# Performance work log

Measured on AMD Instinct MI355X. Metric: run time of the kernel, lower is better.

The kernel has to match this reference:

```python
import jax, jax.numpy as jnp
import numpy as np

B, S, D, A, C, TT, T, NS = 64, 512, 1024, 128, 64, 32, 40, 64
NEG = -1e9


def setup_inputs() -> dict:
    key = jax.random.key(0)
    ks = jax.random.split(key, 24)
    n = lambda k, sh, s: jax.random.normal(k, sh, dtype=jnp.float32) * s
    inp = {
        "encoded_src": n(ks[0], (B, S, D), 1.0),
        "encoded_col": n(ks[1], (B, C, D), 1.0),
        "encoded_tab": n(ks[2], (B, TT, D), 1.0),
        "h0": n(ks[3], (B, D), 1.0),
        "c0": n(ks[4], (B, D), 1.0),
        "action_emb": n(ks[5], (A, D), 0.1),
        "symbol_emb": n(ks[6], (NS, D), 0.1),
        "W_tgt": n(ks[7], (D, D), 0.02), "b_tgt": jnp.zeros((D,), jnp.float32),
        "W_act": n(ks[8], (D, D), 0.02), "b_act": jnp.zeros((D,), jnp.float32),
        "W_col": n(ks[9], (D, D), 0.02), "b_col": jnp.zeros((D,), jnp.float32),
        "W_tab": n(ks[10], (D, D), 0.02), "b_tab": jnp.zeros((D,), jnp.float32),
        "W_out": n(ks[11], (D, D), 0.02), "b_out": jnp.zeros((D,), jnp.float32),
        "W_ih": n(ks[12], (3 * D, 4 * D), 0.02), "b_ih": jnp.zeros((4 * D,), jnp.float32),
        "W_hh": n(ks[13], (D, 4 * D), 0.02), "b_hh": jnp.zeros((4 * D,), jnp.float32),
        "src_mask": jnp.zeros((B, S), jnp.int32),
        "col_mask": jnp.zeros((B, C), jnp.int32),
        "tab_mask": jnp.zeros((B, TT), jnp.int32),
        "action_mask": jnp.zeros((B, A), jnp.int32),
        "cur_node_ids": jax.random.randint(ks[14], (T, B), 0, NS, dtype=jnp.int32),
        "kind": jax.random.randint(ks[15], (T, B), 0, 3, dtype=jnp.int32),
        "gold_idx": jax.random.randint(ks[16], (T, B), 0, TT, dtype=jnp.int32),
    }
    return inp


def reference(encoded_src, encoded_col, encoded_tab, h0, c0, action_emb, symbol_emb,
              W_tgt, b_tgt, W_act, b_act, W_col, b_col, W_tab, b_tab, W_out, b_out,
              W_ih, b_ih, W_hh, b_hh,
              src_mask, col_mask, tab_mask, action_mask, cur_node_ids, kind, gold_idx):
    dt = encoded_src.dtype
    nT, nB = cur_node_ids.shape
    nA = action_emb.shape[0]
    nC = encoded_col.shape[1]
    nTT = encoded_tab.shape[1]
    dim = encoded_src.shape[-1]

    # mask==1 means masked-out (matches torch code: allowed positions set to 0)
    src_bias = jnp.where(src_mask == 1, NEG, 0.0).astype(dt)
    act_bias = jnp.where(action_mask == 1, NEG, 0.0).astype(dt)
    col_bias = jnp.where(col_mask == 1, NEG, 0.0).astype(dt)
    tab_bias = jnp.where(tab_mask == 1, NEG, 0.0).astype(dt)

    # previous-action embedding per step: gather from action table / encoded cols / encoded tabs
    bidx = jnp.arange(nB)
    prev_a = action_emb[gold_idx % nA]                       # [T,B,D]
    prev_c = encoded_col[bidx[None, :], gold_idx % nC]       # [T,B,D]
    prev_t = encoded_tab[bidx[None, :], gold_idx % nTT]      # [T,B,D]
    k3 = kind[..., None]
    prev_sel = jnp.where(k3 == 0, prev_a, jnp.where(k3 == 1, prev_c, prev_t))
    # step 0 uses a zero prev-action embedding
    prev_emb = jnp.concatenate([jnp.zeros((1, nB, dim), dt), prev_sel[:-1]], axis=0)
    node_emb = symbol_emb[cur_node_ids]                      # [T,B,D]

    def step(carry, xs):
        h, c, loss = carry
        pe, ne, kd, gi = xs
        # attention over encoded_src using affine(h) as query
        q = h @ W_tgt + b_tgt                                            # [B,D]
        att = jax.nn.softmax(jnp.einsum('bsd,bd->bs', encoded_src, q) + src_bias, axis=-1)
        ctx = jnp.einsum('bs,bsd->bd', att, encoded_src)                 # [B,D]
        # LSTMCell
        x = jnp.concatenate([pe, ne, ctx], axis=-1)                      # [B,3D]
        gates = x @ W_ih + b_ih + h @ W_hh + b_hh                        # [B,4D]
        i, f, g, o = jnp.split(gates, 4, axis=-1)
        c2 = jax.nn.sigmoid(f) * c + jax.nn.sigmoid(i) * jnp.tanh(g)
        h2 = jax.nn.sigmoid(o) * jnp.tanh(c2)
        out = h2 @ W_out + b_out                                         # [B,D]
        # three prediction heads (action / column / table views)
        la = jax.nn.log_softmax(jnp.einsum('ad,bd->ba', action_emb, out @ W_act + b_act) + act_bias, axis=-1)
        lc = jax.nn.log_softmax(jnp.einsum('bcd,bd->bc', encoded_col, out @ W_col + b_col) + col_bias, axis=-1)
        lt = jax.nn.log_softmax(jnp.einsum('btd,bd->bt', encoded_tab, out @ W_tab + b_tab) + tab_bias, axis=-1)
        ga = jnp.take_along_axis(la, (gi % nA)[:, None], 1)[:, 0]
        gc = jnp.take_along_axis(lc, (gi % nC)[:, None], 1)[:, 0]
        gt = jnp.take_along_axis(lt, (gi % nTT)[:, None], 1)[:, 0]
        lp = jnp.where(kd == 0, ga, jnp.where(kd == 1, gc, gt))
        return (h2, c2, loss - lp), None

    (h, c, loss), _ = jax.lax.scan(step, (h0, c0, jnp.zeros((nB,), dt)),
                                   (prev_emb, node_emb, kind, gold_idx))
    return loss
```

## Files before the change

kernel.cpp:

```cpp
#include <hip/hip_runtime.h>
#include <math.h>

typedef short s8v __attribute__((ext_vector_type(8)));
typedef __bf16 bf8 __attribute__((ext_vector_type(8)));
typedef float f4v __attribute__((ext_vector_type(4)));

#define DEV static __device__ __forceinline__

DEV ushort f2bf(float f){
  union { float f; unsigned u; } v; v.f = f;
  unsigned u = v.u;
  return (ushort)((u + 0x7fffu + ((u>>16)&1u)) >> 16);
}
DEV float bf2f(ushort u){
  union { unsigned u; float f; } v; v.u = ((unsigned)u)<<16; return v.f;
}
DEV float sigm(float x){ return 1.0f/(1.0f + __expf(-x)); }
DEV float tanh_(float x){ float e=__expf(2.f*x); return 1.f - 2.f/(e+1.f); }
DEV float wred(float x){
  #pragma unroll
  for(int off=32; off; off>>=1) x += __shfl_xor(x, off, 64);
  return x;
}
DEV int swz(int row, int uscol){
  return (row<<6) + ((((uscol>>3) ^ (row&7))<<3) | (uscol&7));
}
DEV void gload16(const void* g, void* l){
  __builtin_amdgcn_global_load_lds((const __attribute__((address_space(1))) void*)g,
                                   (__attribute__((address_space(3))) void*)l, 16, 0, 0);
}
DEV int gperm(int n){
  return (((n&1023)>>4)<<6) | ((n>>10)<<4) | (n&15);
}


__global__ void k_cast(const float* __restrict__ s, ushort* __restrict__ d, long n4){
  long i = (long)blockIdx.x*256 + threadIdx.x;
  const long st = (long)gridDim.x*256;
  for(; i<n4; i+=st){
    float4 v = ((const float4*)s)[i];
    ushort4 o; o.x=f2bf(v.x); o.y=f2bf(v.y); o.z=f2bf(v.z); o.w=f2bf(v.w);
    ((ushort4*)d)[i]=o;
  }
}

__global__ __launch_bounds__(256) void k_tr7(const float* __restrict__ wih,
    const float* __restrict__ whh, const float* __restrict__ wtgt,
    const float* __restrict__ wcol, const float* __restrict__ wtab,
    const float* __restrict__ wact, ushort* __restrict__ WihT,
    ushort* __restrict__ WcatT, ushort* __restrict__ WtgtT, ushort* __restrict__ BcatT)
{
  __shared__ ushort T[64][72];
  const int bid = blockIdx.x;
  const float* src; ushort* dst; int C, ldd, roff, cx, ry; bool pm;
  if(bid < 2048){ src=wih; C=4096; dst=WihT; ldd=2048; roff=0; cx=bid&63; ry=bid>>6; pm=true; }
  else if(bid < 3072){ int j=bid-2048; src=wih+2048L*4096; C=4096; dst=WcatT; ldd=2048; roff=0; cx=j&63; ry=j>>6; pm=true; }
  else if(bid < 4096){ int j=bid-3072; src=whh; C=4096; dst=WcatT; ldd=2048; roff=1024; cx=j&63; ry=j>>6; pm=true; }
  else if(bid < 4352){ int j=bid-4096; src=wtgt; C=1024; dst=WtgtT; ldd=1024; roff=0; cx=j&15; ry=j>>4; pm=false; }
  else if(bid < 4608){ int j=bid-4352; src=wcol; C=1024; dst=BcatT; ldd=1024; roff=0; cx=j&15; ry=j>>4; pm=false; }
  else if(bid < 4864){ int j=bid-4608; src=wtab; C=1024; dst=BcatT+1048576; ldd=1024; roff=0; cx=j&15; ry=j>>4; pm=false; }
  else { int j=bid-4864; src=wact; C=1024; dst=BcatT+2097152; ldd=1024; roff=0; cx=j&15; ry=j>>4; pm=false; }
  const int c0 = cx<<6, r0 = ry<<6;
  const int tid = threadIdx.x;
  {
    const int rr = tid>>2, cc = (tid&3)<<4;
    const float* s = src + (long)(r0+rr)*C + c0 + cc;
    float4 v0=*(const float4*)(s), v1=*(const float4*)(s+4), v2=*(const float4*)(s+8), v3=*(const float4*)(s+12);
    ushort* t = &T[rr][cc];
    t[0]=f2bf(v0.x); t[1]=f2bf(v0.y); t[2]=f2bf(v0.z); t[3]=f2bf(v0.w);
    t[4]=f2bf(v1.x); t[5]=f2bf(v1.y); t[6]=f2bf(v1.z); t[7]=f2bf(v1.w);
    t[8]=f2bf(v2.x); t[9]=f2bf(v2.y); t[10]=f2bf(v2.z); t[11]=f2bf(v2.w);
    t[12]=f2bf(v3.x); t[13]=f2bf(v3.y); t[14]=f2bf(v3.z); t[15]=f2bf(v3.w);
  }
  __syncthreads();
  {
    const int rr = tid>>2, cc = (tid&3)<<4;
    s8v o0, o1;
    #pragma unroll
    for(int i=0;i<8;i++){ o0[i]=(short)T[cc+i][rr]; o1[i]=(short)T[cc+8+i][rr]; }
    const int n = c0 + rr;
    const int nr = pm ? gperm(n) : n;
    ushort* dp = dst + (long)nr*ldd + roff + r0 + cc;
    *(s8v*)dp = o0; *(s8v*)(dp+8) = o1;
  }
}

__global__ void k_gatherP(const float* __restrict__ emba, const float* __restrict__ ecol,
                          const float* __restrict__ etab, const float* __restrict__ symb,
                          const int* __restrict__ kindv, const int* __restrict__ gold,
                          const int* __restrict__ cur, ushort* __restrict__ P){
  long i = (long)blockIdx.x*256 + threadIdx.x;
  const long st = (long)gridDim.x*256;
  const long n4 = 2560L*2048/4;
  for(; i<n4; i+=st){
    long pos = i*4; int row = (int)(pos>>11); int col = (int)(pos&2047);
    int t = row>>6, b = row&63;
    ushort4 o;
    if(col < 1024){
      if(t==0){ o.x=o.y=o.z=o.w=0; *(ushort4*)&P[pos]=o; continue; }
      int k = kindv[(t-1)*64+b];
      int gi = gold[(t-1)*64+b];
      const float* s;
      if(k==0) s = emba + ((long)(gi & 127))*1024 + col;
      else if(k==1) s = ecol + (((long)b<<6) + (gi & 63))*1024 + col;
      else s = etab + (((long)b<<5) + (gi & 31))*1024 + col;
      float4 v = *(const float4*)s;
      o.x=f2bf(v.x); o.y=f2bf(v.y); o.z=f2bf(v.z); o.w=f2bf(v.w);
    } else {
      const float* s = symb + ((long)cur[t*64+b])*1024 + (col-1024);
      float4 v = *(const float4*)s;
      o.x=f2bf(v.x); o.y=f2bf(v.y); o.z=f2bf(v.z); o.w=f2bf(v.w);
    }
    *(ushort4*)&P[pos] = o;
  }
}

__global__ void k_init(const float* __restrict__ h0, const float* __restrict__ c0,
                       const float* __restrict__ bih, const float* __restrict__ bhh,
                       const int* __restrict__ smask,
                       float* __restrict__ cbuf, ushort* __restrict__ Ab0,
                       float* __restrict__ biasvec, float* __restrict__ sbias){
  int i = blockIdx.x*256 + threadIdx.x;
  if(i < 65536){
    cbuf[i]=c0[i];
    int row=i>>10, col=i&1023;
    Ab0[(row<<11)+1024+col]=f2bf(h0[i]);
  }
  if(i < 32768) sbias[i] = (smask[i]==1) ? -1.0e9f : 0.f;
  if(i < 4096){
    int nt=i>>6, g=(i>>4)&3, j16=i&15;
    int n = (g<<10) | (nt<<4) | j16;
    biasvec[i] = bih[n] + bhh[n];
  }
}

__global__ void k_bias1(const float* __restrict__ bout,
                        const float* __restrict__ Wa, const float* __restrict__ ba,
                        const float* __restrict__ Wc, const float* __restrict__ bc,
                        const float* __restrict__ Wt, const float* __restrict__ bt,
                        float* __restrict__ vv){
  int j = blockIdx.x*256 + threadIdx.x;
  if(j >= 3072) return;
  int which = j>>10, col = j&1023;
  const float* W = (which==0)?Wa:(which==1)?Wc:Wt;
  const float* bb = (which==0)?ba:(which==1)?bc:bt;
  float s = bb[col];
  for(int i=0;i<1024;i++) s += bout[i]*W[((long)i<<10)+col];
  vv[j] = s;
}

__global__ void k_bias2a(const float* __restrict__ vv, const float* __restrict__ emb,
                         const float* __restrict__ ecol, const float* __restrict__ etab,
                         float* __restrict__ dbuf){
  int wid = blockIdx.x*4 + (threadIdx.x>>6);
  int l = threadIdx.x & 63;
  if(wid >= 6272) return;
  const float* src; const float* v;
  if(wid < 128){ src = emb + ((long)wid<<10); v = vv; }
  else if(wid < 4224){ src = ecol + ((long)(wid-128)<<10); v = vv+1024; }
  else { src = etab + ((long)(wid-4224)<<10); v = vv+2048; }
  const float* sp = src + l*16; const float* vp = v + l*16;
  float s = 0.f;
  #pragma unroll
  for(int i=0;i<16;i+=4){
    float4 a = *(const float4*)(sp+i); float4 bvv = *(const float4*)(vp+i);
    s += a.x*bvv.x + a.y*bvv.y + a.z*bvv.z + a.w*bvv.w;
  }
  s = wred(s);
  if(l==0) dbuf[wid] = s;
}

__global__ void k_bias2b(const float* __restrict__ dbuf,
                         const int* __restrict__ amask, const int* __restrict__ cmask,
                         const int* __restrict__ tmask,
                         float* __restrict__ ca, float* __restrict__ cb, float* __restrict__ ct){
  int i = blockIdx.x*256 + threadIdx.x;
  if(i < 8192){ ca[i] = dbuf[i&127] + ((amask[i]==1)?-1.0e9f:0.f); }
  else if(i < 12288){ int j=i-8192; cb[j] = dbuf[128+j] + ((cmask[j]==1)?-1.0e9f:0.f); }
  else if(i < 14336){ int j=i-12288; ct[j] = dbuf[4224+j] + ((tmask[j]==1)?-1.0e9f:0.f); }
}

template<bool OBF16, bool HASB>
__global__ __launch_bounds__(256,2) void k_gemm128(const ushort* __restrict__ Ap,
    const ushort* __restrict__ Bp, void* __restrict__ Cp, const float* __restrict__ bias,
    int N, int K)
{
  __shared__ __align__(16) ushort As[2][8192];
  __shared__ __align__(16) ushort Bs[2][8192];
  const int tid=threadIdx.x, w=tid>>6, l=tid&63;
  const int wr=w>>1, wc=w&1;
  const int m0=blockIdx.y<<7, n0=blockIdx.x<<7;
  const int lr8 = l>>3, lc = l&7;
  f4v acc[4][4];
  #pragma unroll
  for(int m=0;m<4;m++)
    #pragma unroll
    for(int n=0;n<4;n++) acc[m][n]=(f4v){0.f,0.f,0.f,0.f};

  auto stage=[&](int buf, int k0){
    #pragma unroll
    for(int i=0;i<4;i++){
      const int rb = i*32 + w*8;
      const int row = rb + lr8;
      const int cp = (lc ^ (row&7))<<3;
      gload16(Ap + (long)(m0+row)*K + k0 + cp, &As[buf][rb<<6]);
      gload16(Bp + (long)(n0+row)*K + k0 + cp, &Bs[buf][rb<<6]);
    }
  };
  auto compute=[&](int buf){
    #pragma unroll
    for(int ks=0; ks<2; ks++){
      bf8 av[4], bv[4];
      #pragma unroll
      for(int m=0;m<4;m++){
        const int ar = wr*64 + (m<<4) + (l&15);
        const int ch = (ks<<2) + (l>>4);
        av[m] = *(const bf8*)&As[buf][(ar<<6) + ((ch ^ (ar&7))<<3)];
      }
      #pragma unroll
      for(int n=0;n<4;n++){
        const int br = wc*64 + (n<<4) + (l&15);
        const int ch = (ks<<2) + (l>>4);
        bv[n] = *(const bf8*)&Bs[buf][(br<<6) + ((ch ^ (br&7))<<3)];
      }
      #pragma unroll
      for(int m=0;m<4;m++)
        #pragma unroll
        for(int n=0;n<4;n++)
          acc[m][n] = __builtin_amdgcn_mfma_f32_16x16x32_bf16(av[m], bv[n], acc[m][n], 0,0,0);
    }
  };

  stage(0, 0);
  asm volatile("s_waitcnt vmcnt(0)" ::: "memory");
  __syncthreads();
  int cur=0;
  for(int k0=0;;){
    const int kn = k0+64;
    if(kn<K) stage(cur^1, kn);
    compute(cur);
    asm volatile("s_waitcnt vmcnt(0)" ::: "memory");
    __syncthreads();
    if(kn>=K) break;
    k0=kn; cur^=1;
  }
  #pragma unroll
  for(int m=0;m<4;m++){
    #pragma unroll
    for(int n=0;n<4;n++){
      const int col = n0 + wc*64 + (n<<4) + (l&15);
      float bv_ = 0.f;
      if constexpr(HASB) bv_ = bias[col];
      #pragma unroll
      for(int j=0;j<4;j++){
        const int row = m0 + wr*64 + (m<<4) + ((l>>4)<<2) + j;
        float v = acc[m][n][j] + bv_;
        if constexpr(OBF16) ((ushort*)Cp)[(long)row*N + col] = f2bf(v);
        else ((float*)Cp)[(long)row*N + col] = v;
      }
    }
  }
}

template<bool AF32, bool OBF16, bool HASB>
__global__ __launch_bounds__(256) void k_gemm(const void* __restrict__ Ap,
    const ushort* __restrict__ Bp, void* __restrict__ Cp, const float* __restrict__ bias,
    int M, int N, int K, int lda, int ldb, int ldc, long sAz, long sCz)
{
  __shared__ __align__(16) ushort As[4096];
  __shared__ __align__(16) ushort Bs[4096];
  const int tid=threadIdx.x, w=tid>>6, l=tid&63, q4=l>>4;
  const int r=tid>>2, cc=(tid&3)<<4;
  const int m0=blockIdx.y<<6, n0=blockIdx.x<<6;
  const int z=blockIdx.z;
  f4v acc[4];
  #pragma unroll
  for(int i=0;i<4;i++) acc[i]=(f4v){0.f,0.f,0.f,0.f};

  struct PF { float4 f0,f1,f2,f3; s8v u0,u1,b0,b1; };
  PF pA, pB;

  auto loadAB=[&](int k0, PF& p){
    const int gm = m0 + r;
    if constexpr(AF32){
      if(gm < M){
        const float* a = (const float*)Ap + sAz*z + (long)gm*lda + k0 + cc;
        p.f0=*(const float4*)(a); p.f1=*(const float4*)(a+4); p.f2=*(const float4*)(a+8); p.f3=*(const float4*)(a+12);
      } else { p.f0=p.f1=p.f2=p.f3=make_float4(0.f,0.f,0.f,0.f); }
    } else {
      if(gm < M){
        const ushort* a = (const ushort*)Ap + sAz*z + (long)gm*lda + k0 + cc;
        p.u0=*(const s8v*)a; p.u1=*(const s8v*)(a+8);
      } else { p.u0=p.u1=(s8v){0,0,0,0,0,0,0,0}; }
    }
    const ushort* b = Bp + (long)(n0+r)*ldb + k0 + cc;
    p.b0=*(const s8v*)b; p.b1=*(const s8v*)(b+8);
  };
  auto stage=[&](const PF& p){
    s8v a0, a1;
    if constexpr(AF32){
      a0[0]=(short)f2bf(p.f0.x); a0[1]=(short)f2bf(p.f0.y); a0[2]=(short)f2bf(p.f0.z); a0[3]=(short)f2bf(p.f0.w);
      a0[4]=(short)f2bf(p.f1.x); a0[5]=(short)f2bf(p.f1.y); a0[6]=(short)f2bf(p.f1.z); a0[7]=(short)f2bf(p.f1.w);
      a1[0]=(short)f2bf(p.f2.x); a1[1]=(short)f2bf(p.f2.y); a1[2]=(short)f2bf(p.f2.z); a1[3]=(short)f2bf(p.f2.w);
      a1[4]=(short)f2bf(p.f3.x); a1[5]=(short)f2bf(p.f3.y); a1[6]=(short)f2bf(p.f3.z); a1[7]=(short)f2bf(p.f3.w);
    } else { a0=p.u0; a1=p.u1; }
    *(s8v*)&As[swz(r,cc)] = a0; *(s8v*)&As[swz(r,cc+8)] = a1;
    *(s8v*)&Bs[swz(r,cc)] = p.b0; *(s8v*)&Bs[swz(r,cc+8)] = p.b1;
  };
  auto compute=[&](){
    #pragma unroll
    for(int ks=0; ks<64; ks+=32){
      bf8 av = *(const bf8*)&As[swz((w<<4)+(l&15), ks+(q4<<3))];
      #pragma unroll
      for(int nf=0; nf<4; nf++){
        bf8 bv = *(const bf8*)&Bs[swz((nf<<4)+(l&15), ks+(q4<<3))];
        acc[nf] = __builtin_amdgcn_mfma_f32_16x16x32_bf16(av, bv, acc[nf], 0, 0, 0);
      }
    }
  };

  loadAB(0, pA); loadAB(64, pB);
  for(int k0=0; k0<K; k0+=128){
    stage(pA); __syncthreads();
    if(k0+128 < K) loadAB(k0+128, pA);
    compute(); __syncthreads();
    stage(pB); __syncthreads();
    if(k0+192 < K) loadAB(k0+192, pB);
    compute(); __syncthreads();
  }
  #pragma unroll
  for(int nf=0; nf<4; nf++){
    const int col = n0 + (nf<<4) + (l&15);
    float bv = 0.f;
    if constexpr(HASB) bv = bias[col];
    #pragma unroll
    for(int j=0;j<4;j++){
      const int row = m0 + (w<<4) + ((l>>4)<<2) + j;
      if(row < M){
        float v = acc[nf][j] + bv;
        if constexpr(OBF16) ((ushort*)Cp)[sCz*z + (long)row*ldc + col] = f2bf(v);
        else ((float*)Cp)[sCz*z + (long)row*ldc + col] = v;
      }
    }
  }
}


__global__ __launch_bounds__(256) void k_attn(const ushort* __restrict__ esrc,
    const float* __restrict__ q, const float* __restrict__ sbias,
    float* __restrict__ pm, float* __restrict__ pl, float* __restrict__ pctx)
{
  const int b = blockIdx.x>>4, j = blockIdx.x&15;
  const int tid = threadIdx.x, w = tid>>6, l = tid&63;
  __shared__ float ms[4], ls[4];
  __shared__ float ctxs[4][1024];
  float qr[16];
  {
    const float* qp = q + (b<<10) + (l<<4);
    #pragma unroll
    for(int i=0;i<16;i+=4){ float4 v=*(const float4*)(qp+i); qr[i]=v.x; qr[i+1]=v.y; qr[i+2]=v.z; qr[i+3]=v.w; }
  }
  float m = -3.4e38f, lsum = 0.f;
  float cacc[16];
  #pragma unroll
  for(int i=0;i<16;i++) cacc[i]=0.f;
  const int sbase = (j<<5) + w;
  for(int rr=0; rr<8; rr++){
    const int s = sbase + (rr<<2);
    const ushort* ep = esrc + (((long)((b<<9) + s))<<10) + (l<<4);
    s8v e0 = *(const s8v*)ep, e1 = *(const s8v*)(ep+8);
    float ef[16];
    #pragma unroll
    for(int i=0;i<8;i++){ ef[i]=bf2f((ushort)e0[i]); ef[8+i]=bf2f((ushort)e1[i]); }
    float d = 0.f;
    #pragma unroll
    for(int i=0;i<16;i++) d += ef[i]*qr[i];
    d = wred(d);
    d += sbias[(b<<9)+s];
    const float mn = fmaxf(m, d);
    const float sc = __expf(m - mn);
    const float p = __expf(d - mn);
    lsum = lsum*sc + p;
    #pragma unroll
    for(int i=0;i<16;i++) cacc[i] = cacc[i]*sc + p*ef[i];
    m = mn;
  }
  if(l==0){ ms[w]=m; ls[w]=lsum; }
  #pragma unroll
  for(int i=0;i<16;i++) ctxs[w][(l<<4)+i]=cacc[i];
  __syncthreads();
  const float mb = fmaxf(fmaxf(ms[0],ms[1]),fmaxf(ms[2],ms[3]));
  const float w0=__expf(ms[0]-mb), w1=__expf(ms[1]-mb), w2=__expf(ms[2]-mb), w3=__expf(ms[3]-mb);
  const float lb = ls[0]*w0 + ls[1]*w1 + ls[2]*w2 + ls[3]*w3;
  const int jb = (j<<6) + b;
  float* pc = pctx + ((long)jb<<10);
  for(int d0=tid; d0<1024; d0+=256){
    pc[d0] = ctxs[0][d0]*w0 + ctxs[1][d0]*w1 + ctxs[2][d0]*w2 + ctxs[3][d0]*w3;
  }
  if(tid==0){ pm[jb]=mb; pl[jb]=lb; }
}

__global__ __launch_bounds__(256) void k_combine(const float* __restrict__ pm,
    const float* __restrict__ pl, const float* __restrict__ pctx, ushort* __restrict__ Ab)
{
  const int idx = blockIdx.x*256 + threadIdx.x;
  const int b = idx>>7, c0 = (idx&127)<<3;
  float mv[16];
  #pragma unroll
  for(int j=0;j<16;j++) mv[j] = pm[(j<<6)+b];
  float M = mv[0];
  #pragma unroll
  for(int j=1;j<16;j++) M = fmaxf(M, mv[j]);
  float e[16]; float den = 0.f;
  #pragma unroll
  for(int j=0;j<16;j++){ e[j] = __expf(mv[j]-M); den += pl[(j<<6)+b]*e[j]; }
  const float inv = 1.f/den;
  float s0=0,s1=0,s2=0,s3=0,s4=0,s5=0,s6=0,s7=0;
  #pragma unroll
  for(int j=0;j<16;j++){
    const float wj = e[j]*inv;
    const float* p = pctx + (((long)((j<<6)+b))<<10) + c0;
    float4 v0=*(const float4*)p, v1=*(const float4*)(p+4);
    s0+=wj*v0.x; s1+=wj*v0.y; s2+=wj*v0.z; s3+=wj*v0.w;
    s4+=wj*v1.x; s5+=wj*v1.y; s6+=wj*v1.z; s7+=wj*v1.w;
  }
  s8v o;
  o[0]=(short)f2bf(s0); o[1]=(short)f2bf(s1); o[2]=(short)f2bf(s2); o[3]=(short)f2bf(s3);
  o[4]=(short)f2bf(s4); o[5]=(short)f2bf(s5); o[6]=(short)f2bf(s6); o[7]=(short)f2bf(s7);
  *(s8v*)&Ab[(b<<11)+c0] = o;
}

__global__ __launch_bounds__(256) void k_lstm(const ushort* __restrict__ Abuf,
    const float* __restrict__ cin, const ushort* __restrict__ WcatP,
    const ushort* __restrict__ gpre_t, float* __restrict__ cout,
    ushort* __restrict__ AbOut, ushort* __restrict__ h2t)
{
  __shared__ __align__(16) ushort As[4096];
  __shared__ __align__(16) ushort Bs[4096];
  const int tid=threadIdx.x, w=tid>>6, l=tid&63, q4=l>>4, l15=l&15;
  const int r=tid>>2, cc=(tid&3)<<4;
  const int nt = blockIdx.x;
  f4v acc[4];
  #pragma unroll
  for(int nf=0;nf<4;nf++){
    #pragma unroll
    for(int jj=0;jj<4;jj++){
      const int row = (w<<4) + ((l>>4)<<2) + jj;
      acc[nf][jj] = bf2f(gpre_t[((long)row<<12) + (nt<<6) + (nf<<4) + l15]);
    }
  }
  struct PF { s8v a0,a1,b0,b1; };
  PF pA, pB;
  auto loadAB=[&](int k0, PF& p){
    const ushort* a = Abuf + ((long)r<<11) + k0 + cc;
    p.a0=*(const s8v*)a; p.a1=*(const s8v*)(a+8);
    const ushort* bp = WcatP + ((long)((nt<<6)+r)<<11) + k0 + cc;
    p.b0=*(const s8v*)bp; p.b1=*(const s8v*)(bp+8);
  };
  auto stage=[&](const PF& p){
    *(s8v*)&As[swz(r,cc)] = p.a0; *(s8v*)&As[swz(r,cc+8)] = p.a1;
    *(s8v*)&Bs[swz(r,cc)] = p.b0; *(s8v*)&Bs[swz(r,cc+8)] = p.b1;
  };
  auto compute=[&](){
    #pragma unroll
    for(int ks=0; ks<64; ks+=32){
      bf8 av = *(const bf8*)&As[swz((w<<4)+l15, ks+(q4<<3))];
      #pragma unroll
      for(int nf=0;nf<4;nf++){
        bf8 bv = *(const bf8*)&Bs[swz((nf<<4)+l15, ks+(q4<<3))];
        acc[nf] = __builtin_amdgcn_mfma_f32_16x16x32_bf16(av, bv, acc[nf], 0, 0, 0);
      }
    }
  };
  loadAB(0, pA); loadAB(64, pB);
  for(int k0=0; k0<2048; k0+=128){
    stage(pA); __syncthreads();
    if(k0+128 < 2048) loadAB(k0+128, pA);
    compute(); __syncthreads();
    stage(pB); __syncthreads();
    if(k0+192 < 2048) loadAB(k0+192, pB);
    compute(); __syncthreads();
  }
  #pragma unroll
  for(int jj=0;jj<4;jj++){
    const int row = (w<<4) + ((l>>4)<<2) + jj;
    const int j = (nt<<4) + l15;
    const float iv = acc[0][jj], fv = acc[1][jj], gv = acc[2][jj], ov = acc[3][jj];
    const float cold = cin[(row<<10)+j];
    const float c2 = sigm(fv)*cold + sigm(iv)*tanh_(gv);
    const float h2v = sigm(ov)*tanh_(c2);
    cout[(row<<10)+j] = c2;
    const ushort hb = f2bf(h2v);
    AbOut[(row<<11) + 1024 + j] = hb;
    h2t[(row<<10)+j] = hb;
  }
}

__global__ __launch_bounds__(256) void k_loss(const ushort* __restrict__ h2a,
    const ushort* __restrict__ GAt, const ushort* __restrict__ GCt, const ushort* __restrict__ GTt,
    const float* __restrict__ ca, const float* __restrict__ cb, const float* __restrict__ ct,
    const int* __restrict__ gold, const int* __restrict__ kindv, float* __restrict__ lossbuf)
{
  const int blk = blockIdx.x;
  const int t = blk/192, rem = blk - t*192;
  const int b = rem/3, head = rem - b*3;
  const int tid = threadIdx.x, w = tid>>6, l = tid&63;
  __shared__ float logits[128];
  int R; const ushort* G; const float* cons;
  if(head==0){ R=128; G=GAt; cons=ca + (b<<7); }
  else if(head==1){ R=64; G=GCt + ((long)b<<16); cons=cb + (b<<6); }
  else { R=32; G=GTt + ((long)b<<15); cons=ct + (b<<5); }
  float hr[16];
  {
    const ushort* hp = h2a + (((long)((t<<6)+b))<<10) + l*16;
    s8v h0v=*(const s8v*)hp, h1v=*(const s8v*)(hp+8);
    #pragma unroll
    for(int i=0;i<8;i++){ hr[i]=bf2f((ushort)h0v[i]); hr[8+i]=bf2f((ushort)h1v[i]); }
  }
  for(int rr=w; rr<R; rr+=4){
    const ushort* gp = G + ((long)rr<<10) + l*16;
    s8v g0=*(const s8v*)gp, g1=*(const s8v*)(gp+8);
    float d = 0.f;
    #pragma unroll
    for(int i=0;i<8;i++){ d += bf2f((ushort)g0[i])*hr[i]; d += bf2f((ushort)g1[i])*hr[8+i]; }
    d = wred(d);
    if(l==0) logits[rr] = d + cons[rr];
  }
  __syncthreads();
  if(w==0){
    float mx = -3.4e38f;
    for(int idx=l; idx<R; idx+=64) mx = fmaxf(mx, logits[idx]);
    #pragma unroll
    for(int off=32; off; off>>=1) mx = fmaxf(mx, __shfl_xor(mx, off, 64));
    float s = 0.f;
    for(int idx=l; idx<R; idx+=64) s += __expf(logits[idx]-mx);
    s = wred(s);
    if(l==0){
      const float lse = mx + __logf(s);
      const int kd = kindv[(t<<6)+b];
      const bool mine = (head==0 && kd==0) || (head==1 && kd==1) || (head==2 && kd>=2);
      if(mine){
        const int gi = gold[(t<<6)+b];
        lossbuf[(t<<6)+b] = logits[gi & (R-1)] - lse;
      }
    }
  }
}

__global__ void k_loss_fin(const float* __restrict__ lossbuf, float* __restrict__ out){
  int b = threadIdx.x;
  if(b < 64){
    float s = 0.f;
    for(int t=0;t<40;t++) s += lossbuf[(t<<6)+b];
    out[b] = -s;
  }
}


extern "C" void kernel_launch(void* const* d_in, const int* in_sizes, int n_in,
                              void* d_out, int out_size, void* d_ws, size_t ws_size,
                              hipStream_t stream)
{
  const float *e_src=(const float*)d_in[0], *e_col=(const float*)d_in[1], *e_tab=(const float*)d_in[2];
  const float *h0=(const float*)d_in[3], *c0=(const float*)d_in[4];
  const float *emba=(const float*)d_in[5], *embs=(const float*)d_in[6];
  const float *W_tgt=(const float*)d_in[7], *b_tgt=(const float*)d_in[8];
  const float *W_act=(const float*)d_in[9], *b_act=(const float*)d_in[10];
  const float *W_col=(const float*)d_in[11], *b_col=(const float*)d_in[12];
  const float *W_tab=(const float*)d_in[13], *b_tab=(const float*)d_in[14];
  const float *W_out=(const float*)d_in[15], *b_out=(const float*)d_in[16];
  const float *W_ih=(const float*)d_in[17], *b_ih=(const float*)d_in[18];
  const float *W_hh=(const float*)d_in[19], *b_hh=(const float*)d_in[20];
  const int *smask=(const int*)d_in[21], *cmask=(const int*)d_in[22], *tmask=(const int*)d_in[23];
  const int *amask=(const int*)d_in[24];
  const int *cur=(const int*)d_in[25], *kindp=(const int*)d_in[26], *goldp=(const int*)d_in[27];

  char* wp = (char*)d_ws;
  auto alloc = [&](size_t n)->char*{ char* p = wp; wp += (n + 255) & ~(size_t)255; return p; };
  ushort* esrc_bf = (ushort*)alloc(67108864);
  ushort* WihT    = (ushort*)alloc(16777216);
  ushort* WcatP   = (ushort*)alloc(16777216);
  ushort* WtgtT   = (ushort*)alloc(2097152);
  ushort* BcatT   = (ushort*)alloc(6291456);
  ushort* Woutb   = (ushort*)alloc(2097152);
  float*  U       = (float*) alloc(12582912);
  ushort* Ubf     = (ushort*)alloc(6291456);
  ushort* GAt     = (ushort*)alloc(262144);
  ushort* GCt     = (ushort*)alloc(8388608);
  ushort* GTt     = (ushort*)alloc(4194304);
  ushort* gpre    = (ushort*)alloc(20971520);
  float* biasvec  = (float*)alloc(16384);
  float* sbias    = (float*)alloc(131072);
  float* vv       = (float*)alloc(12288);
  float* dbuf     = (float*)alloc(25088);
  float* ca       = (float*)alloc(32768);
  float* cb       = (float*)alloc(16384);
  float* ctb      = (float*)alloc(8192);
  float* pm       = (float*)alloc(4096);
  float* pl       = (float*)alloc(4096);
  float* pctx     = (float*)alloc(4194304);
  ushort* Ab0     = (ushort*)alloc(262144);
  ushort* Ab1     = (ushort*)alloc(262144);
  float* cbuf0    = (float*)alloc(262144);
  float* cbuf1    = (float*)alloc(262144);
  float* qb       = (float*)alloc(262144);
  ushort* h2a     = (ushort*)alloc(5242880);
  float* lossbuf  = (float*)alloc(10240);
  ushort* P       = (ushort*)U;
  float* out      = (float*)d_out;

  k_cast<<<4096,256,0,stream>>>(e_src, esrc_bf, 8388608L);
  k_cast<<<512,256,0,stream>>>(W_out, Woutb, 262144L);
  k_tr7<<<5120,256,0,stream>>>(W_ih, W_hh, W_tgt, W_col, W_tab, W_act,
                               WihT, WcatP, WtgtT, BcatT);
  k_init<<<256,256,0,stream>>>(h0, c0, b_ih, b_hh, smask, cbuf0, Ab0, biasvec, sbias);

  { dim3 g(24,8); k_gemm128<false,false><<<g,256,0,stream>>>(Woutb, BcatT, U, nullptr, 3072, 1024); }
  k_cast<<<1024,256,0,stream>>>(U, Ubf, 786432L);
  { dim3 g(16,2); k_gemm<true,true,false><<<g,256,0,stream>>>(emba, Ubf+2048, GAt, nullptr,
        128,1024,1024, 1024,3072,1024, 0,0); }
  { dim3 g(16,1,64); k_gemm<true,true,false><<<g,256,0,stream>>>(e_col, Ubf, GCt, nullptr,
        64,1024,1024, 1024,3072,1024, 65536,65536); }
  { dim3 g(16,1,64); k_gemm<true,true,false><<<g,256,0,stream>>>(e_tab, Ubf+1024, GTt, nullptr,
        32,1024,1024, 1024,3072,1024, 32768,32768); }
  k_bias1<<<12,256,0,stream>>>(b_out, W_act, b_act, W_col, b_col, W_tab, b_tab, vv);
  k_bias2a<<<1568,256,0,stream>>>(vv, emba, e_col, e_tab, dbuf);
  k_bias2b<<<56,256,0,stream>>>(dbuf, amask, cmask, tmask, ca, cb, ctb);

  k_gatherP<<<2048,256,0,stream>>>(emba, e_col, e_tab, embs, kindp, goldp, cur, P);
  { dim3 g(32,20); k_gemm128<true,true><<<g,256,0,stream>>>(P, WihT, gpre, biasvec, 4096, 2048); }
  { dim3 g(16,1); k_gemm<true,false,true><<<g,256,0,stream>>>(h0, WtgtT, qb, b_tgt,
        64,1024,1024, 1024,1024,1024, 0,0); }

  for(int t=0; t<40; t++){
    ushort* Ain  = (t&1) ? Ab1 : Ab0;
    ushort* Aout = (t&1) ? Ab0 : Ab1;
    float* ci = (t&1) ? cbuf1 : cbuf0;
    float* co = (t&1) ? cbuf0 : cbuf1;
    k_attn<<<1024,256,0,stream>>>(esrc_bf, qb, sbias, pm, pl, pctx);
    k_combine<<<32,256,0,stream>>>(pm, pl, pctx, Ain);
    k_lstm<<<64,256,0,stream>>>(Ain, ci, WcatP, gpre + (long)t*262144, co, Aout, h2a + (long)t*65536);
    { dim3 g(16,1); k_gemm<false,false,true><<<g,256,0,stream>>>(Aout + 1024, WtgtT, qb, b_tgt,
          64,1024,1024, 2048,1024,1024, 0,0); }
  }
  k_loss<<<7680,256,0,stream>>>(h2a, GAt, GCt, GTt, ca, cb, ctb, goldp, kindp, lossbuf);
  k_loss_fin<<<1,64,0,stream>>>(lossbuf, out);
}
```

Baseline: 2.140 ms.

## Compute loss logits with MFMA GEMMs and parallelize bias projection

The per-(t,b,head) loss kernel, which did wave-level dot products over all three heads for every step, is replaced by batched GEMMs: one GEMM for the action logits and per-batch GEMMs for the column and table logits. A light softmax kernel then handles only the head selected by kind. The k_bias1 kernel, which looped serially over 1024 inputs per thread, is rewritten to use one wave per output and read the already-transposed bf16 weights. The GEMM gains a B stride, and the tab logits buffer is padded to 64 rows so the table head works with 64-wide tiles.

```diff
diff --git a/kernel.cpp b/kernel.cpp
--- a/kernel.cpp
+++ b/kernel.cpp
@@ -134,19 +134,29 @@
   }
 }
 
-__global__ void k_bias1(const float* __restrict__ bout,
-                        const float* __restrict__ Wa, const float* __restrict__ ba,
-                        const float* __restrict__ Wc, const float* __restrict__ bc,
-                        const float* __restrict__ Wt, const float* __restrict__ bt,
-                        float* __restrict__ vv){
-  int j = blockIdx.x*256 + threadIdx.x;
-  if(j >= 3072) return;
-  int which = j>>10, col = j&1023;
-  const float* W = (which==0)?Wa:(which==1)?Wc:Wt;
-  const float* bb = (which==0)?ba:(which==1)?bc:bt;
-  float s = bb[col];
-  for(int i=0;i<1024;i++) s += bout[i]*W[((long)i<<10)+col];
-  vv[j] = s;
+__global__ __launch_bounds__(256) void k_bias1b(const float* __restrict__ bout,
+    const ushort* __restrict__ BcatT, const float* __restrict__ ba,
+    const float* __restrict__ bc, const float* __restrict__ bt,
+    float* __restrict__ vv)
+{
+  const int wid = blockIdx.x*4 + (threadIdx.x>>6);
+  const int l = threadIdx.x & 63;
+  const int which = wid>>10, col = wid&1023;
+  const ushort* W = (which==0) ? (BcatT + 2097152)
+                  : (which==1) ? BcatT
+                               : (BcatT + 1048576);
+  const float bb = ((which==0)?ba:(which==1)?bc:bt)[col];
+  const ushort* wp = W + (long)col*1024 + l*16;
+  const float* bp = bout + l*16;
+  s8v w0 = *(const s8v*)wp, w1 = *(const s8v*)(wp+8);
+  float s = 0.f;
+  #pragma unroll
+  for(int i=0;i<8;i++){
+    s += bf2f((ushort)w0[i]) * bp[i];
+    s += bf2f((ushort)w1[i]) * bp[8+i];
+  }
+  s = wred(s);
+  if(l==0) vv[wid] = bb + s;
 }
 
 __global__ void k_bias2a(const float* __restrict__ vv, const float* __restrict__ emb,
@@ -265,7 +275,7 @@
 template<bool AF32, bool OBF16, bool HASB>
 __global__ __launch_bounds__(256) void k_gemm(const void* __restrict__ Ap,
     const ushort* __restrict__ Bp, void* __restrict__ Cp, const float* __restrict__ bias,
-    int M, int N, int K, int lda, int ldb, int ldc, long sAz, long sCz)
+    int M, int N, int K, int lda, int ldb, int ldc, long sAz, long sBz, long sCz)
 {
   __shared__ __align__(16) ushort As[4096];
   __shared__ __align__(16) ushort Bs[4096];
@@ -293,7 +303,7 @@
         p.u0=*(const s8v*)a; p.u1=*(const s8v*)(a+8);
       } else { p.u0=p.u1=(s8v){0,0,0,0,0,0,0,0}; }
     }
-    const ushort* b = Bp + (long)(n0+r)*ldb + k0 + cc;
+    const ushort* b = Bp + sBz*z + (long)(n0+r)*ldb + k0 + cc;
     p.b0=*(const s8v*)b; p.b1=*(const s8v*)(b+8);
   };
   auto stage=[&](const PF& p){
@@ -496,55 +506,30 @@
   }
 }
 
-__global__ __launch_bounds__(256) void k_loss(const ushort* __restrict__ h2a,
-    const ushort* __restrict__ GAt, const ushort* __restrict__ GCt, const ushort* __restrict__ GTt,
+__global__ __launch_bounds__(256) void k_loss2(const float* __restrict__ la,
+    const float* __restrict__ lcb, const float* __restrict__ ltb,
     const float* __restrict__ ca, const float* __restrict__ cb, const float* __restrict__ ct,
     const int* __restrict__ gold, const int* __restrict__ kindv, float* __restrict__ lossbuf)
 {
-  const int blk = blockIdx.x;
-  const int t = blk/192, rem = blk - t*192;
-  const int b = rem/3, head = rem - b*3;
-  const int tid = threadIdx.x, w = tid>>6, l = tid&63;
-  __shared__ float logits[128];
-  int R; const ushort* G; const float* cons;
-  if(head==0){ R=128; G=GAt; cons=ca + (b<<7); }
-  else if(head==1){ R=64; G=GCt + ((long)b<<16); cons=cb + (b<<6); }
-  else { R=32; G=GTt + ((long)b<<15); cons=ct + (b<<5); }
-  float hr[16];
-  {
-    const ushort* hp = h2a + (((long)((t<<6)+b))<<10) + l*16;
-    s8v h0v=*(const s8v*)hp, h1v=*(const s8v*)(hp+8);
-    #pragma unroll
-    for(int i=0;i<8;i++){ hr[i]=bf2f((ushort)h0v[i]); hr[8+i]=bf2f((ushort)h1v[i]); }
-  }
-  for(int rr=w; rr<R; rr+=4){
-    const ushort* gp = G + ((long)rr<<10) + l*16;
-    s8v g0=*(const s8v*)gp, g1=*(const s8v*)(gp+8);
-    float d = 0.f;
-    #pragma unroll
-    for(int i=0;i<8;i++){ d += bf2f((ushort)g0[i])*hr[i]; d += bf2f((ushort)g1[i])*hr[8+i]; }
-    d = wred(d);
-    if(l==0) logits[rr] = d + cons[rr];
-  }
-  __syncthreads();
-  if(w==0){
-    float mx = -3.4e38f;
-    for(int idx=l; idx<R; idx+=64) mx = fmaxf(mx, logits[idx]);
-    #pragma unroll
-    for(int off=32; off; off>>=1) mx = fmaxf(mx, __shfl_xor(mx, off, 64));
-    float s = 0.f;
-    for(int idx=l; idx<R; idx+=64) s += __expf(logits[idx]-mx);
-    s = wred(s);
-    if(l==0){
-      const float lse = mx + __logf(s);
-      const int kd = kindv[(t<<6)+b];
-      const bool mine = (head==0 && kd==0) || (head==1 && kd==1) || (head==2 && kd>=2);
-      if(mine){
-        const int gi = gold[(t<<6)+b];
-        lossbuf[(t<<6)+b] = logits[gi & (R-1)] - lse;
-      }
-    }
-  }
+  const int wv = threadIdx.x>>6, l = threadIdx.x&63;
+  const int tb = blockIdx.x*4 + wv;
+  const int t = tb>>6, b = tb&63;
+  const int kd = kindv[tb];
+  const int gi = gold[tb];
+  const float* ptr; const float* cons; int R;
+  if(kd==0){ ptr = la + (long)tb*128; cons = ca + (b<<7); R=128; }
+  else if(kd==1){ ptr = lcb + (long)b*2560 + t*64; cons = cb + (b<<6); R=64; }
+  else { ptr = ltb + (long)b*2560 + t*64; cons = ct + (b<<5); R=32; }
+  const int gidx = gi & (R-1);
+  const float v  = (l < R) ? (ptr[l] + cons[l]) : -3.4e38f;
+  const float v2 = (R==128) ? (ptr[l+64] + cons[l+64]) : -3.4e38f;
+  float mx = fmaxf(v, v2);
+  #pragma unroll
+  for(int off=32; off; off>>=1) mx = fmaxf(mx, __shfl_xor(mx, off, 64));
+  float s = ((l<R)?__expf(v-mx):0.f) + ((R==128)?__expf(v2-mx):0.f);
+  s = wred(s);
+  const float gv = ptr[gidx] + cons[gidx];
+  if(l==0) lossbuf[tb] = gv - (mx + __logf(s));
 }
 
 __global__ void k_loss_fin(const float* __restrict__ lossbuf, float* __restrict__ out){
@@ -587,7 +572,7 @@
   ushort* Ubf     = (ushort*)alloc(6291456);
   ushort* GAt     = (ushort*)alloc(262144);
   ushort* GCt     = (ushort*)alloc(8388608);
-  ushort* GTt     = (ushort*)alloc(4194304);
+  ushort* GTt     = (ushort*)alloc(8388608);
   ushort* gpre    = (ushort*)alloc(20971520);
   float* biasvec  = (float*)alloc(16384);
   float* sbias    = (float*)alloc(131072);
@@ -605,6 +590,9 @@
   float* cbuf1    = (float*)alloc(262144);
   float* qb       = (float*)alloc(262144);
   ushort* h2a     = (ushort*)alloc(5242880);
+  float* la       = (float*)alloc(1310720);
+  float* lcb      = (float*)alloc(655360);
+  float* ltb      = (float*)alloc(655360);
   float* lossbuf  = (float*)alloc(10240);
   ushort* P       = (ushort*)U;
   float* out      = (float*)d_out;
@@ -618,19 +606,19 @@
   { dim3 g(24,8); k_gemm128<false,false><<<g,256,0,stream>>>(Woutb, BcatT, U, nullptr, 3072, 1024); }
   k_cast<<<1024,256,0,stream>>>(U, Ubf, 786432L);
   { dim3 g(16,2); k_gemm<true,true,false><<<g,256,0,stream>>>(emba, Ubf+2048, GAt, nullptr,
-        128,1024,1024, 1024,3072,1024, 0,0); }
+        128,1024,1024, 1024,3072,1024, 0,0,0); }
   { dim3 g(16,1,64); k_gemm<true,true,false><<<g,256,0,stream>>>(e_col, Ubf, GCt, nullptr,
-        64,1024,1024, 1024,3072,1024, 65536,65536); }
+        64,1024,1024, 1024,3072,1024, 65536,0,65536); }
   { dim3 g(16,1,64); k_gemm<true,true,false><<<g,256,0,stream>>>(e_tab, Ubf+1024, GTt, nullptr,
-        32,1024,1024, 1024,3072,1024, 32768,32768); }
-  k_bias1<<<12,256,0,stream>>>(b_out, W_act, b_act, W_col, b_col, W_tab, b_tab, vv);
+        32,1024,1024, 1024,3072,1024, 32768,0,65536); }
+  k_bias1b<<<768,256,0,stream>>>(b_out, BcatT, b_act, b_col, b_tab, vv);
   k_bias2a<<<1568,256,0,stream>>>(vv, emba, e_col, e_tab, dbuf);
   k_bias2b<<<56,256,0,stream>>>(dbuf, amask, cmask, tmask, ca, cb, ctb);
 
   k_gatherP<<<2048,256,0,stream>>>(emba, e_col, e_tab, embs, kindp, goldp, cur, P);
   { dim3 g(32,20); k_gemm128<true,true><<<g,256,0,stream>>>(P, WihT, gpre, biasvec, 4096, 2048); }
   { dim3 g(16,1); k_gemm<true,false,true><<<g,256,0,stream>>>(h0, WtgtT, qb, b_tgt,
-        64,1024,1024, 1024,1024,1024, 0,0); }
+        64,1024,1024, 1024,1024,1024, 0,0,0); }
 
   for(int t=0; t<40; t++){
     ushort* Ain  = (t&1) ? Ab1 : Ab0;
@@ -641,8 +629,14 @@
     k_combine<<<32,256,0,stream>>>(pm, pl, pctx, Ain);
     k_lstm<<<64,256,0,stream>>>(Ain, ci, WcatP, gpre + (long)t*262144, co, Aout, h2a + (long)t*65536);
     { dim3 g(16,1); k_gemm<false,false,true><<<g,256,0,stream>>>(Aout + 1024, WtgtT, qb, b_tgt,
-          64,1024,1024, 2048,1024,1024, 0,0); }
-  }
-  k_loss<<<7680,256,0,stream>>>(h2a, GAt, GCt, GTt, ca, cb, ctb, goldp, kindp, lossbuf);
+          64,1024,1024, 2048,1024,1024, 0,0,0); }
+  }
+
+  { dim3 g(1,20); k_gemm128<false,false><<<g,256,0,stream>>>(h2a, GAt, la, nullptr, 128, 1024); }
+  { dim3 g(1,1,64); k_gemm<false,false,false><<<g,256,0,stream>>>(h2a, GCt, lcb, nullptr,
+        40,64,1024, 65536,1024,64, 1024,65536,2560); }
+  { dim3 g(1,1,64); k_gemm<false,false,false><<<g,256,0,stream>>>(h2a, GTt, ltb, nullptr,
+        40,64,1024, 65536,1024,64, 1024,65536,2560); }
+  k_loss2<<<640,256,0,stream>>>(la, lcb, ltb, ca, cb, ctb, goldp, kindp, lossbuf);
   k_loss_fin<<<1,64,0,stream>>>(lossbuf, out);
 }
```

Measured after the change: 2.083 ms (median of 2 runs). 1.03x faster.
